# Kernel tuning notes

Measured on AMD Instinct MI355X. Metric: run time of the kernel, lower is better.

Reference implementation:

```python
import jax, jax.numpy as jnp
import numpy as np

B, N, C, H = 4, 2048, 1024, 16
HD = C // H  # head dim = 64


def setup_inputs() -> dict:
    key = jax.random.key(0)
    k1, k2, k3, k4 = jax.random.split(key, 4)
    x = jax.random.normal(k1, (B, N, C), dtype=jnp.float32)
    # nn.Linear(C, 3C, bias=False): weight [3C, C], y = x @ W.T
    w_qkv = jax.random.normal(k2, (3 * C, C), dtype=jnp.float32) * (C ** -0.5)
    # nn.Linear(C, C) with bias
    w_out = jax.random.normal(k3, (C, C), dtype=jnp.float32) * (C ** -0.5)
    b_out = jax.random.normal(k4, (C,), dtype=jnp.float32) * 0.01
    return {"x": x, "w_qkv": w_qkv, "w_out": w_out, "b_out": b_out}


def reference(x, w_qkv, w_out, b_out):
    scale = HD ** -0.5
    qkv = jnp.einsum('bnc,dc->bnd', x, w_qkv)  # [B, N, 3C]
    q, k, v = jnp.split(qkv, 3, axis=-1)
    # rearrange 'b n (h c) -> b h n c'
    def heads(t):
        return t.reshape(B, N, H, HD).transpose(0, 2, 1, 3)
    q, k, v = heads(q) * scale, heads(k), heads(v)
    scores = jnp.einsum('bhnc,bhmc->bhnm', q, k)  # [B, H, N, N]
    attn = jax.nn.softmax(scores, axis=-1)
    v_hat = jnp.einsum('bhnm,bhmc->bhnc', attn, v)
    out = v_hat.transpose(0, 2, 1, 3).reshape(B, N, C)  # 'b h n c -> b n (h c)'
    return jnp.einsum('bnc,dc->bnd', out, w_out) + b_out
```

## Files before the change

### kernel.cpp

```cpp
#include <hip/hip_runtime.h>

typedef unsigned short ushort_t;
typedef __attribute__((ext_vector_type(8))) short short8;
typedef __attribute__((ext_vector_type(4))) float f32x4;
typedef __attribute__((ext_vector_type(16))) float f32x16;
typedef __attribute__((ext_vector_type(4))) float float4v;
typedef __attribute__((ext_vector_type(4))) unsigned short ushortx4;
typedef __attribute__((ext_vector_type(4))) unsigned int uint4v;

#define AS1 __attribute__((address_space(1)))
#define AS3 __attribute__((address_space(3)))

#define B_ 4
#define N_ 2048
#define C_ 1024
#define H_ 16
#define HD_ 64
#define M_TOT 8192
#define N3_ 3072

#define QSCALE 0.18033688011112042f

__device__ __forceinline__ unsigned short f2bf(float f) {
    unsigned int u = __float_as_uint(f);
    u += 0x7fffu + ((u >> 16) & 1u);
    return (unsigned short)(u >> 16);
}

__global__ __launch_bounds__(256) void cast3_f32_bf16(const float* __restrict__ xa,
                                                      const float* __restrict__ xb,
                                                      const float* __restrict__ xc,
                                                      ushort_t* __restrict__ oa,
                                                      ushort_t* __restrict__ ob,
                                                      ushort_t* __restrict__ oc,
                                                      int n4a, int n4b, int n4c) {
    int i = blockIdx.x * blockDim.x + threadIdx.x;
    const int stride = gridDim.x * blockDim.x;
    const int tot = n4a + n4b + n4c;
    for (; i < tot; i += stride) {
        const float4v* src;
        ushortx4* dst;
        int j = i;
        if (j < n4a) { src = (const float4v*)xa; dst = (ushortx4*)oa; }
        else if ((j -= n4a) < n4b) { src = (const float4v*)xb; dst = (ushortx4*)ob; }
        else { j -= n4b; src = (const float4v*)xc; dst = (ushortx4*)oc; }
        float4v v = src[j];
        ushortx4 o;
        o[0] = f2bf(v[0]); o[1] = f2bf(v[1]); o[2] = f2bf(v[2]); o[3] = f2bf(v[3]);
        dst[j] = o;
    }
}


template <int EPI>
__global__ __launch_bounds__(512, 2) void gemm8p(const ushort_t* __restrict__ A,
                                                 const ushort_t* __restrict__ Bw,
                                                 ushort_t* __restrict__ o0,
                                                 ushort_t* __restrict__ o1,
                                                 ushort_t* __restrict__ o2,
                                                 float* __restrict__ outf,
                                                 const float* __restrict__ bias,
                                                 int K, int NBX) {
    extern __shared__ ushort_t smem[];
    const int tid = threadIdx.x;
    const int lane = tid & 63;
    const int wid = tid >> 6;
    const int l15 = lane & 15, lg = lane >> 4;
    const int wr = wid >> 1;
    const int wc = wid & 1;

    const int wg = blockIdx.x;
    const int id = (wg & 7) * ((int)gridDim.x >> 3) + (wg >> 3);
    const int by = id / NBX, bx = id - by * NBX;
    const int m0 = by * 256, n0 = bx * 128;

    const int koff = (((lane >> 4) ^ ((lane >> 1) & 3)) << 3);
    const int trow = tid >> 2;
    const int slotsrc = (tid & 3) ^ ((tid >> 3) & 3);

    auto stageA = [&](int q, int tt, int kh, int c) {
        const ushort_t* src = A + (size_t)(m0 + c * 128 + trow) * K + tt * 64 + kh * 32 +
                              slotsrc * 8;
        ushort_t* dst = smem + q * 24576 + kh * 8192 + c * 4096 + tid * 8;
        __builtin_amdgcn_global_load_lds((const AS1 void*)src, (AS3 void*)dst, 16, 0, 0);
    };
    auto stageB = [&](int q, int tt, int kh) {
        const ushort_t* src = Bw + (size_t)(n0 + trow) * K + tt * 64 + kh * 32 + slotsrc * 8;
        ushort_t* dst = smem + q * 24576 + 16384 + kh * 4096 + tid * 8;
        __builtin_amdgcn_global_load_lds((const AS1 void*)src, (AS3 void*)dst, 16, 0, 0);
    };

    f32x4 acc[4][4] = {};

    auto phase = [&](int p, int kh) {
        const ushort_t* Ab = smem + p * 24576 + kh * 8192;
        const ushort_t* Bb = smem + p * 24576 + 16384 + kh * 4096;
        short8 af[4], bfr[4];
#pragma unroll
        for (int rt = 0; rt < 4; ++rt)
            af[rt] = *(const short8*)(Ab + (wr * 64 + rt * 16 + l15) * 32 + koff);
#pragma unroll
        for (int ni = 0; ni < 4; ++ni)
            bfr[ni] = *(const short8*)(Bb + (wc * 64 + ni * 16 + l15) * 32 + koff);
        __builtin_amdgcn_s_setprio(1);
#pragma unroll
        for (int rt = 0; rt < 4; ++rt)
#pragma unroll
            for (int ni = 0; ni < 4; ++ni)
                acc[rt][ni] = __builtin_amdgcn_mfma_f32_16x16x32_bf16(af[rt], bfr[ni],
                                                                      acc[rt][ni], 0, 0, 0);
        __builtin_amdgcn_s_setprio(0);
    };

    stageA(0, 0, 0, 0); stageA(0, 0, 0, 1);
    stageA(0, 0, 1, 0); stageA(0, 0, 1, 1);
    stageB(0, 0, 0);    stageB(0, 0, 1);

    const int NT = K >> 6;
    for (int t = 0; t < NT; ++t) {
        const int p = t & 1, q = p ^ 1;
        if (t + 1 < NT) {
            stageA(q, t + 1, 0, 0); stageA(q, t + 1, 0, 1);
            __builtin_amdgcn_sched_barrier(0);
            asm volatile("s_waitcnt vmcnt(2)");
        } else {
            asm volatile("s_waitcnt vmcnt(0)");
        }
        __builtin_amdgcn_sched_barrier(0);
        __builtin_amdgcn_s_barrier();
        __builtin_amdgcn_sched_barrier(0);
        phase(p, 0);
        if (t + 1 < NT) {
            stageA(q, t + 1, 1, 0); stageA(q, t + 1, 1, 1);
            stageB(q, t + 1, 0);    stageB(q, t + 1, 1);
        }
        __builtin_amdgcn_sched_barrier(0);
        __builtin_amdgcn_s_barrier();
        __builtin_amdgcn_sched_barrier(0);
        phase(p, 1);
    }

    if (EPI == 0) {
        const int sel = bx >> 3;
#pragma unroll
        for (int mi = 0; mi < 4; ++mi) {
            const int r0 = m0 + wr * 64 + mi * 16 + lg * 4;
            const int b = r0 >> 11, n = r0 & 2047;
            const int blk = n >> 5, nlo = n & 31;
#pragma unroll
            for (int ni = 0; ni < 4; ++ni) {
                const int cq = (bx & 7) * 128 + wc * 64 + ni * 16 + l15;
                const int h = cq >> 6, hd = cq & 63;
                const int bh = b * H_ + h;
                f32x4 a = acc[mi][ni];
                if (sel == 2) {
                    size_t base = (((size_t)(bh * 64 + blk) * 2 + (hd >> 5)) * 2 +
                                   ((n >> 4) & 1)) * 512 +
                                  ((hd & 31) + ((n >> 3) & 1) * 32) * 8 + (n & 7);
                    ushortx4 pk;
#pragma unroll
                    for (int j = 0; j < 4; ++j) pk[j] = f2bf(a[j]);
                    *(ushortx4*)(&o2[base]) = pk;
                } else {
                    size_t base = ((size_t)(bh * 64 + blk) * 4 + (hd >> 4)) * 512 +
                                  (nlo + ((hd >> 3) & 1) * 32) * 8 + (hd & 7);
                    if (sel == 0) {
#pragma unroll
                        for (int j = 0; j < 4; ++j) o0[base + j * 8] = f2bf(a[j] * QSCALE);
                    } else {
#pragma unroll
                        for (int j = 0; j < 4; ++j) o1[base + j * 8] = f2bf(a[j]);
                    }
                }
            }
        }
    } else {
#pragma unroll
        for (int ni = 0; ni < 4; ++ni) {
            const int c = n0 + wc * 64 + ni * 16 + l15;
            const float bv = bias[c];
#pragma unroll
            for (int mi = 0; mi < 4; ++mi) {
                const int r0 = m0 + wr * 64 + mi * 16 + lg * 4;
                f32x4 a = acc[mi][ni];
#pragma unroll
                for (int j = 0; j < 4; ++j)
                    outf[(size_t)(r0 + j) * C_ + c] = a[j] + bv;
            }
        }
    }
}

__global__ __launch_bounds__(256, 2) void attn_fwd(const ushort_t* __restrict__ Qf,
                                                   const ushort_t* __restrict__ Kf,
                                                   const ushort_t* __restrict__ Vf,
                                                   ushort_t* __restrict__ Ov) {
    const int tid = threadIdx.x;
    const int lane = tid & 63;
    const int wid = tid >> 6;
    const int lc = lane & 31, lh = lane >> 5;

    const int wg = blockIdx.x;
    const int xcd = wg & 7, slot = wg >> 3;
    const int bh = xcd * 8 + (slot >> 3);
    const int qt = slot & 7;

    const ushort_t* qpb = Qf + (size_t)bh * N_ * HD_;
    const ushort_t* kpb = Kf + (size_t)bh * N_ * HD_;
    const ushort_t* vpb = Vf + (size_t)bh * N_ * HD_;

    const int qblk0 = qt * 8 + wid * 2;

    short8 qf[2][4];
#pragma unroll
    for (int qc = 0; qc < 2; ++qc)
#pragma unroll
        for (int ks = 0; ks < 4; ++ks)
            qf[qc][ks] = *(const short8*)(qpb + ((size_t)(qblk0 + qc) * 4 + ks) * 512 +
                                          lane * 8);

    f32x16 oacc[2][2] = {};
    float srun[2] = {0.f, 0.f};

    short8 kfA[4], kfB[4], vfA[4], vfB[4];
#pragma unroll
    for (int ks = 0; ks < 4; ++ks)
        kfA[ks] = *(const short8*)(kpb + (size_t)ks * 512 + lane * 8);
#pragma unroll
    for (int dt = 0; dt < 2; ++dt)
#pragma unroll
        for (int kb = 0; kb < 2; ++kb)
            vfA[dt * 2 + kb] = *(const short8*)(vpb + ((size_t)dt * 2 + kb) * 512 + lane * 8);

    auto iter = [&](short8(&kfu)[4], short8(&kfp)[4], short8(&vfu)[4], short8(&vfp)[4],
                    int t) {
        f32x16 sacc[2] = {};
        __builtin_amdgcn_s_setprio(1);
#pragma unroll
        for (int qc = 0; qc < 2; ++qc)
#pragma unroll
            for (int ks = 0; ks < 4; ++ks)
                sacc[qc] = __builtin_amdgcn_mfma_f32_32x32x16_bf16(kfu[ks], qf[qc][ks],
                                                                   sacc[qc], 0, 0, 0);
        __builtin_amdgcn_s_setprio(0);

        const int kvn = (t + 1) & 63;
#pragma unroll
        for (int ks = 0; ks < 4; ++ks)
            kfp[ks] = *(const short8*)(kpb + ((size_t)kvn * 4 + ks) * 512 + lane * 8);
#pragma unroll
        for (int dt = 0; dt < 2; ++dt)
#pragma unroll
            for (int kb = 0; kb < 2; ++kb)
                vfp[dt * 2 + kb] = *(const short8*)(vpb + (((size_t)kvn * 2 + dt) * 2 + kb) *
                                                    512 + lane * 8);

#pragma unroll
        for (int qc = 0; qc < 2; ++qc) {
            float p[16];
#pragma unroll
            for (int r = 0; r < 16; ++r) p[r] = __builtin_amdgcn_exp2f(sacc[qc][r]);
            float s01 = (p[0] + p[1]) + (p[2] + p[3]);
            float s23 = (p[4] + p[5]) + (p[6] + p[7]);
            float s45 = (p[8] + p[9]) + (p[10] + p[11]);
            float s67 = (p[12] + p[13]) + (p[14] + p[15]);
            srun[qc] += (s01 + s23) + (s45 + s67);

            unsigned pk[4][2];
#pragma unroll
            for (int r1 = 0; r1 < 4; ++r1)
#pragma unroll
                for (int c = 0; c < 2; ++c)
                    asm("v_cvt_pk_bf16_f32 %0, %1, %2"
                        : "=v"(pk[r1][c])
                        : "v"(p[4 * r1 + 2 * c]), "v"(p[4 * r1 + 2 * c + 1]));

            short8 pb[2];
#pragma unroll
            for (int kb = 0; kb < 2; ++kb) {
                unsigned a0 = pk[2 * kb][0], b0 = pk[2 * kb + 1][0];
                unsigned a1 = pk[2 * kb][1], b1 = pk[2 * kb + 1][1];
                asm("v_permlane32_swap_b32 %0, %1" : "+v"(a0), "+v"(b0));
                asm("v_permlane32_swap_b32 %0, %1" : "+v"(a1), "+v"(b1));
                uint4v w;
                w[0] = a0; w[1] = a1; w[2] = b0; w[3] = b1;
                pb[kb] = __builtin_bit_cast(short8, w);
            }

            __builtin_amdgcn_s_setprio(1);
#pragma unroll
            for (int dt = 0; dt < 2; ++dt)
#pragma unroll
                for (int kb = 0; kb < 2; ++kb)
                    oacc[qc][dt] = __builtin_amdgcn_mfma_f32_32x32x16_bf16(
                        vfu[dt * 2 + kb], pb[kb], oacc[qc][dt], 0, 0, 0);
            __builtin_amdgcn_s_setprio(0);
        }
    };

    for (int t2 = 0; t2 < 64; t2 += 2) {
        iter(kfA, kfB, vfA, vfB, t2);
        iter(kfB, kfA, vfB, vfA, t2 + 1);
    }

    const int b = bh >> 4, h = bh & 15;
#pragma unroll
    for (int qc = 0; qc < 2; ++qc) {
        float s = srun[qc];
        s += __shfl_xor(s, 32, 64);
        const float inv = 1.f / s;
        const int qg = (qblk0 + qc) * 32 + lc;
        ushort_t* orow = Ov + (size_t)(b * N_ + qg) * C_ + h * HD_;
#pragma unroll
        for (int dt = 0; dt < 2; ++dt)
#pragma unroll
            for (int r1 = 0; r1 < 4; ++r1) {
                ushortx4 pkv;
#pragma unroll
                for (int r0 = 0; r0 < 4; ++r0)
                    pkv[r0] = f2bf(oacc[qc][dt][4 * r1 + r0] * inv);
                *(ushortx4*)(orow + dt * 32 + r1 * 8 + lh * 4) = pkv;
            }
    }
}

extern "C" void kernel_launch(void* const* d_in, const int* in_sizes, int n_in,
                              void* d_out, int out_size, void* d_ws, size_t ws_size,
                              hipStream_t stream) {
    const float* x = (const float*)d_in[0];
    const float* wqkv = (const float*)d_in[1];
    const float* wout = (const float*)d_in[2];
    const float* bout = (const float*)d_in[3];
    float* out = (float*)d_out;

    ushort_t* ws = (ushort_t*)d_ws;
    const size_t XN = (size_t)M_TOT * C_;
    const size_t WQN = (size_t)N3_ * C_;
    const size_t WON = (size_t)C_ * C_;
    ushort_t* xbf = ws;
    ushort_t* wqkvb = xbf + XN;
    ushort_t* woutb = wqkvb + WQN;
    ushort_t* karr = woutb + WON;
    ushort_t* varr = karr + XN;
    ushort_t* qarr = varr + XN;
    ushort_t* vhat = xbf;

    cast3_f32_bf16<<<2048, 256, 0, stream>>>(x, wqkv, wout, xbf, wqkvb, woutb,
                                             (int)(XN / 4), (int)(WQN / 4), (int)(WON / 4));

    gemm8p<0><<<768, 512, 98304, stream>>>(xbf, wqkvb, qarr, karr, varr,
                                           nullptr, nullptr, C_, 24);
    attn_fwd<<<512, 256, 0, stream>>>(qarr, karr, varr, vhat);
    gemm8p<1><<<256, 512, 98304, stream>>>(vhat, woutb, nullptr, nullptr, nullptr,
                                           out, bout, C_, 8);
}
```

Baseline: 176.9 us.

## Fuse fp32-to-bf16 conversion of x into QKV GEMM A-tile staging

The QKV GEMM now reads fp32 x directly through register loads, converts it to bf16 with v_cvt_pk_bf16_f32, and writes swizzled tiles into LDS. This removes the separate cast pass over x and its bf16 round trip through global memory. The cast kernel now handles only the weights. In exchange the A operand no longer uses the async global_load_lds path: it reads twice the bytes per tile, each tile is loaded by all 24 N-blocks, and the pipeline has one barrier per k-step with a full vmcnt wait.

```diff
diff --git a/kernel.cpp b/kernel.cpp
--- a/kernel.cpp
+++ b/kernel.cpp
@@ -6,6 +6,7 @@
 typedef __attribute__((ext_vector_type(16))) float f32x16;
 typedef __attribute__((ext_vector_type(4))) float float4v;
 typedef __attribute__((ext_vector_type(4))) unsigned short ushortx4;
+typedef __attribute__((ext_vector_type(2))) unsigned int uint2v;
 typedef __attribute__((ext_vector_type(4))) unsigned int uint4v;
 
 #define AS1 __attribute__((address_space(1)))
@@ -27,22 +28,19 @@
     return (unsigned short)(u >> 16);
 }
 
-__global__ __launch_bounds__(256) void cast3_f32_bf16(const float* __restrict__ xa,
-                                                      const float* __restrict__ xb,
+__global__ __launch_bounds__(256) void cast2_f32_bf16(const float* __restrict__ xb,
                                                       const float* __restrict__ xc,
-                                                      ushort_t* __restrict__ oa,
                                                       ushort_t* __restrict__ ob,
                                                       ushort_t* __restrict__ oc,
-                                                      int n4a, int n4b, int n4c) {
+                                                      int n4b, int n4c) {
     int i = blockIdx.x * blockDim.x + threadIdx.x;
     const int stride = gridDim.x * blockDim.x;
-    const int tot = n4a + n4b + n4c;
+    const int tot = n4b + n4c;
     for (; i < tot; i += stride) {
         const float4v* src;
         ushortx4* dst;
         int j = i;
-        if (j < n4a) { src = (const float4v*)xa; dst = (ushortx4*)oa; }
-        else if ((j -= n4a) < n4b) { src = (const float4v*)xb; dst = (ushortx4*)ob; }
+        if (j < n4b) { src = (const float4v*)xb; dst = (ushortx4*)ob; }
         else { j -= n4b; src = (const float4v*)xc; dst = (ushortx4*)oc; }
         float4v v = src[j];
         ushortx4 o;
@@ -52,8 +50,8 @@
 }
 
 
-template <int EPI>
-__global__ __launch_bounds__(512, 2) void gemm8p(const ushort_t* __restrict__ A,
+template <int EPI, int AF32>
+__global__ __launch_bounds__(512, 2) void gemm8p(const void* __restrict__ Avoid,
                                                  const ushort_t* __restrict__ Bw,
                                                  ushort_t* __restrict__ o0,
                                                  ushort_t* __restrict__ o1,
@@ -62,6 +60,8 @@
                                                  const float* __restrict__ bias,
                                                  int K, int NBX) {
     extern __shared__ ushort_t smem[];
+    const ushort_t* A = (const ushort_t*)Avoid;
+    const float* Af = (const float*)Avoid;
     const int tid = threadIdx.x;
     const int lane = tid & 63;
     const int wid = tid >> 6;
@@ -78,7 +78,13 @@
     const int trow = tid >> 2;
     const int slotsrc = (tid & 3) ^ ((tid >> 3) & 3);
 
-    auto stageA = [&](int q, int tt, int kh, int c) {
+    const int wrow0 = wid * 32 + (lane >> 4);
+    const int acol = (lane & 15) * 4;
+    const int akh = (lane >> 3) & 1;
+    const int aslot = (lane & 7) >> 1;
+    const int ae = (lane & 1) * 4;
+
+    auto stageAbf = [&](int q, int tt, int kh, int c) {
         const ushort_t* src = A + (size_t)(m0 + c * 128 + trow) * K + tt * 64 + kh * 32 +
                               slotsrc * 8;
         ushort_t* dst = smem + q * 24576 + kh * 8192 + c * 4096 + tid * 8;
@@ -89,6 +95,14 @@
         ushort_t* dst = smem + q * 24576 + 16384 + kh * 4096 + tid * 8;
         __builtin_amdgcn_global_load_lds((const AS1 void*)src, (AS3 void*)dst, 16, 0, 0);
     };
+    auto writeA = [&](int q, const float4v& av, int j) {
+        uint2v w;
+        asm("v_cvt_pk_bf16_f32 %0, %1, %2" : "=v"(w[0]) : "v"(av[0]), "v"(av[1]));
+        asm("v_cvt_pk_bf16_f32 %0, %1, %2" : "=v"(w[1]) : "v"(av[2]), "v"(av[3]));
+        const int rj = wrow0 + j * 4;
+        const int dsv = aslot ^ ((rj >> 1) & 3);
+        *(uint2v*)(smem + q * 24576 + akh * 8192 + rj * 32 + dsv * 8 + ae) = w;
+    };
 
     f32x4 acc[4][4] = {};
 
@@ -112,32 +126,71 @@
         __builtin_amdgcn_s_setprio(0);
     };
 
-    stageA(0, 0, 0, 0); stageA(0, 0, 0, 1);
-    stageA(0, 0, 1, 0); stageA(0, 0, 1, 1);
-    stageB(0, 0, 0);    stageB(0, 0, 1);
-
     const int NT = K >> 6;
-    for (int t = 0; t < NT; ++t) {
-        const int p = t & 1, q = p ^ 1;
-        if (t + 1 < NT) {
-            stageA(q, t + 1, 0, 0); stageA(q, t + 1, 0, 1);
+
+    if constexpr (AF32) {
+        {
+            const float* as0 = Af + (size_t)(m0 + wrow0) * K + acol;
+            float4v av[8];
+#pragma unroll
+            for (int j = 0; j < 8; ++j) av[j] = *(const float4v*)(as0 + (size_t)(j * 4) * K);
+            stageB(0, 0, 0); stageB(0, 0, 1);
+#pragma unroll
+            for (int j = 0; j < 8; ++j) writeA(0, av[j], j);
+        }
+        __syncthreads();
+        for (int t = 0; t < NT; ++t) {
+            const int p = t & 1, q = p ^ 1;
+            const bool more = (t + 1 < NT);
+            float4v av[8];
+            if (more) {
+                const float* asrc = Af + (size_t)(m0 + wrow0) * K + (t + 1) * 64 + acol;
+#pragma unroll
+                for (int j = 0; j < 8; ++j)
+                    av[j] = *(const float4v*)(asrc + (size_t)(j * 4) * K);
+                stageB(q, t + 1, 0); stageB(q, t + 1, 1);
+            }
+            phase(p, 0);
+            if (more) {
+#pragma unroll
+                for (int j = 0; j < 8; ++j) writeA(q, av[j], j);
+            }
+            phase(p, 1);
+            if (more) {
+                __builtin_amdgcn_sched_barrier(0);
+                asm volatile("s_waitcnt vmcnt(0) lgkmcnt(0)");
+                __builtin_amdgcn_sched_barrier(0);
+                __builtin_amdgcn_s_barrier();
+                __builtin_amdgcn_sched_barrier(0);
+            }
+        }
+    } else {
+        stageAbf(0, 0, 0, 0); stageAbf(0, 0, 0, 1);
+        stageAbf(0, 0, 1, 0); stageAbf(0, 0, 1, 1);
+        stageB(0, 0, 0);      stageB(0, 0, 1);
+        __syncthreads();
+        for (int t = 0; t < NT; ++t) {
+            const int p = t & 1, q = p ^ 1;
+            if (t + 1 < NT) {
+                stageAbf(q, t + 1, 0, 0); stageAbf(q, t + 1, 0, 1);
+                __builtin_amdgcn_sched_barrier(0);
+                asm volatile("s_waitcnt vmcnt(2)");
+            } else {
+                asm volatile("s_waitcnt vmcnt(0)");
+            }
             __builtin_amdgcn_sched_barrier(0);
-            asm volatile("s_waitcnt vmcnt(2)");
-        } else {
-            asm volatile("s_waitcnt vmcnt(0)");
-        }
-        __builtin_amdgcn_sched_barrier(0);
-        __builtin_amdgcn_s_barrier();
-        __builtin_amdgcn_sched_barrier(0);
-        phase(p, 0);
-        if (t + 1 < NT) {
-            stageA(q, t + 1, 1, 0); stageA(q, t + 1, 1, 1);
-            stageB(q, t + 1, 0);    stageB(q, t + 1, 1);
-        }
-        __builtin_amdgcn_sched_barrier(0);
-        __builtin_amdgcn_s_barrier();
-        __builtin_amdgcn_sched_barrier(0);
-        phase(p, 1);
+            __builtin_amdgcn_s_barrier();
+            __builtin_amdgcn_sched_barrier(0);
+            phase(p, 0);
+            if (t + 1 < NT) {
+                stageAbf(q, t + 1, 1, 0); stageAbf(q, t + 1, 1, 1);
+                stageB(q, t + 1, 0);      stageB(q, t + 1, 1);
+            }
+            __builtin_amdgcn_sched_barrier(0);
+            __builtin_amdgcn_s_barrier();
+            __builtin_amdgcn_sched_barrier(0);
+            phase(p, 1);
+        }
     }
 
     if (EPI == 0) {
@@ -337,20 +390,19 @@
     const size_t XN = (size_t)M_TOT * C_;
     const size_t WQN = (size_t)N3_ * C_;
     const size_t WON = (size_t)C_ * C_;
-    ushort_t* xbf = ws;
-    ushort_t* wqkvb = xbf + XN;
+    ushort_t* wqkvb = ws;
     ushort_t* woutb = wqkvb + WQN;
     ushort_t* karr = woutb + WON;
     ushort_t* varr = karr + XN;
     ushort_t* qarr = varr + XN;
-    ushort_t* vhat = xbf;
-
-    cast3_f32_bf16<<<2048, 256, 0, stream>>>(x, wqkv, wout, xbf, wqkvb, woutb,
-                                             (int)(XN / 4), (int)(WQN / 4), (int)(WON / 4));
-
-    gemm8p<0><<<768, 512, 98304, stream>>>(xbf, wqkvb, qarr, karr, varr,
-                                           nullptr, nullptr, C_, 24);
+    ushort_t* vhat = qarr + XN;
+
+    cast2_f32_bf16<<<512, 256, 0, stream>>>(wqkv, wout, wqkvb, woutb,
+                                            (int)(WQN / 4), (int)(WON / 4));
+
+    gemm8p<0, 1><<<768, 512, 98304, stream>>>(x, wqkvb, qarr, karr, varr,
+                                              nullptr, nullptr, C_, 24);
     attn_fwd<<<512, 256, 0, stream>>>(qarr, karr, varr, vhat);
-    gemm8p<1><<<256, 512, 98304, stream>>>(vhat, woutb, nullptr, nullptr, nullptr,
-                                           out, bout, C_, 8);
+    gemm8p<1, 0><<<256, 512, 98304, stream>>>(vhat, woutb, nullptr, nullptr, nullptr,
+                                              out, bout, C_, 8);
 }
```

Result: slower. 196.7 us (+11.2%).

## Triple-buffer GEMM LDS stages with two-tile prefetch and finer interleaved phases

Applied to the files above, without the earlier changes.

Rewrites the bf16 GEMM main loop to use three LDS stages, prefetching two K-tiles ahead instead of one. Each K-tile is split into four sub-phases, with global-to-LDS loads interleaved between LDS fragment reads and MFMA groups. The aim is to hide global memory latency more fully. LDS use grows to 144 KB per block, which likely prevents two blocks from sharing a CU and reduces occupancy. The extra barriers also add synchronization cost.

```diff
diff --git a/kernel.cpp b/kernel.cpp
--- a/kernel.cpp
+++ b/kernel.cpp
@@ -53,7 +53,7 @@
 
 
 template <int EPI>
-__global__ __launch_bounds__(512, 2) void gemm8p(const ushort_t* __restrict__ A,
+__global__ __launch_bounds__(512, 2) void gemm8f(const ushort_t* __restrict__ A,
                                                  const ushort_t* __restrict__ Bw,
                                                  ushort_t* __restrict__ o0,
                                                  ushort_t* __restrict__ o1,
@@ -89,55 +89,124 @@
         ushort_t* dst = smem + q * 24576 + 16384 + kh * 4096 + tid * 8;
         __builtin_amdgcn_global_load_lds((const AS1 void*)src, (AS3 void*)dst, 16, 0, 0);
     };
+    auto stage6 = [&](int q, int tt) {
+        stageA(q, tt, 0, 0); stageA(q, tt, 0, 1);
+        stageA(q, tt, 1, 0); stageA(q, tt, 1, 1);
+        stageB(q, tt, 0);    stageB(q, tt, 1);
+    };
 
     f32x4 acc[4][4] = {};
 
-    auto phase = [&](int p, int kh) {
-        const ushort_t* Ab = smem + p * 24576 + kh * 8192;
-        const ushort_t* Bb = smem + p * 24576 + 16384 + kh * 4096;
-        short8 af[4], bfr[4];
-#pragma unroll
-        for (int rt = 0; rt < 4; ++rt)
-            af[rt] = *(const short8*)(Ab + (wr * 64 + rt * 16 + l15) * 32 + koff);
-#pragma unroll
-        for (int ni = 0; ni < 4; ++ni)
-            bfr[ni] = *(const short8*)(Bb + (wc * 64 + ni * 16 + l15) * 32 + koff);
-        __builtin_amdgcn_s_setprio(1);
-#pragma unroll
-        for (int rt = 0; rt < 4; ++rt)
-#pragma unroll
-            for (int ni = 0; ni < 4; ++ni)
-                acc[rt][ni] = __builtin_amdgcn_mfma_f32_16x16x32_bf16(af[rt], bfr[ni],
-                                                                      acc[rt][ni], 0, 0, 0);
-        __builtin_amdgcn_s_setprio(0);
-    };
-
-    stageA(0, 0, 0, 0); stageA(0, 0, 0, 1);
-    stageA(0, 0, 1, 0); stageA(0, 0, 1, 1);
-    stageB(0, 0, 0);    stageB(0, 0, 1);
+    auto rdA = [&](const ushort_t* base, int kh, int rt) -> short8 {
+        return *(const short8*)(base + kh * 8192 + (wr * 64 + rt * 16 + l15) * 32 + koff);
+    };
+    auto rdB = [&](const ushort_t* base, int kh, int ni) -> short8 {
+        return *(const short8*)(base + 16384 + kh * 4096 + (wc * 64 + ni * 16 + l15) * 32 +
+                                koff);
+    };
+
+    stage6(0, 0);
+    stage6(1, 1);
 
     const int NT = K >> 6;
+    int cur = 0;
     for (int t = 0; t < NT; ++t) {
-        const int p = t & 1, q = p ^ 1;
+        const int nxt = (cur + 2 >= 3) ? cur - 1 : cur + 2;
+        const bool pf = (t + 2 < NT);
+
         if (t + 1 < NT) {
-            stageA(q, t + 1, 0, 0); stageA(q, t + 1, 0, 1);
-            __builtin_amdgcn_sched_barrier(0);
-            asm volatile("s_waitcnt vmcnt(2)");
+            asm volatile("s_waitcnt vmcnt(6)");
         } else {
             asm volatile("s_waitcnt vmcnt(0)");
         }
         __builtin_amdgcn_sched_barrier(0);
         __builtin_amdgcn_s_barrier();
         __builtin_amdgcn_sched_barrier(0);
-        phase(p, 0);
-        if (t + 1 < NT) {
-            stageA(q, t + 1, 1, 0); stageA(q, t + 1, 1, 1);
-            stageB(q, t + 1, 0);    stageB(q, t + 1, 1);
-        }
-        __builtin_amdgcn_sched_barrier(0);
-        __builtin_amdgcn_s_barrier();
-        __builtin_amdgcn_sched_barrier(0);
-        phase(p, 1);
+
+        const ushort_t* base = smem + cur * 24576;
+        short8 a0, a1, bfr[4];
+
+        a0 = rdA(base, 0, 0); a1 = rdA(base, 0, 1);
+#pragma unroll
+        for (int ni = 0; ni < 4; ++ni) bfr[ni] = rdB(base, 0, ni);
+        if (pf) { stageA(nxt, t + 2, 0, 0); stageA(nxt, t + 2, 0, 1); }
+        __builtin_amdgcn_sched_barrier(0);
+        __builtin_amdgcn_s_barrier();
+        asm volatile("s_waitcnt lgkmcnt(0)");
+        __builtin_amdgcn_sched_barrier(0);
+        __builtin_amdgcn_s_setprio(1);
+#pragma unroll
+        for (int ni = 0; ni < 4; ++ni)
+            acc[0][ni] = __builtin_amdgcn_mfma_f32_16x16x32_bf16(a0, bfr[ni], acc[0][ni],
+                                                                 0, 0, 0);
+#pragma unroll
+        for (int ni = 0; ni < 4; ++ni)
+            acc[1][ni] = __builtin_amdgcn_mfma_f32_16x16x32_bf16(a1, bfr[ni], acc[1][ni],
+                                                                 0, 0, 0);
+        __builtin_amdgcn_s_setprio(0);
+        __builtin_amdgcn_sched_barrier(0);
+        __builtin_amdgcn_s_barrier();
+
+        a0 = rdA(base, 0, 2); a1 = rdA(base, 0, 3);
+        if (pf) stageB(nxt, t + 2, 0);
+        __builtin_amdgcn_sched_barrier(0);
+        __builtin_amdgcn_s_barrier();
+        asm volatile("s_waitcnt lgkmcnt(0)");
+        __builtin_amdgcn_sched_barrier(0);
+        __builtin_amdgcn_s_setprio(1);
+#pragma unroll
+        for (int ni = 0; ni < 4; ++ni)
+            acc[2][ni] = __builtin_amdgcn_mfma_f32_16x16x32_bf16(a0, bfr[ni], acc[2][ni],
+                                                                 0, 0, 0);
+#pragma unroll
+        for (int ni = 0; ni < 4; ++ni)
+            acc[3][ni] = __builtin_amdgcn_mfma_f32_16x16x32_bf16(a1, bfr[ni], acc[3][ni],
+                                                                 0, 0, 0);
+        __builtin_amdgcn_s_setprio(0);
+        __builtin_amdgcn_sched_barrier(0);
+        __builtin_amdgcn_s_barrier();
+
+        a0 = rdA(base, 1, 0); a1 = rdA(base, 1, 1);
+#pragma unroll
+        for (int ni = 0; ni < 4; ++ni) bfr[ni] = rdB(base, 1, ni);
+        if (pf) { stageA(nxt, t + 2, 1, 0); stageA(nxt, t + 2, 1, 1); }
+        __builtin_amdgcn_sched_barrier(0);
+        __builtin_amdgcn_s_barrier();
+        asm volatile("s_waitcnt lgkmcnt(0)");
+        __builtin_amdgcn_sched_barrier(0);
+        __builtin_amdgcn_s_setprio(1);
+#pragma unroll
+        for (int ni = 0; ni < 4; ++ni)
+            acc[0][ni] = __builtin_amdgcn_mfma_f32_16x16x32_bf16(a0, bfr[ni], acc[0][ni],
+                                                                 0, 0, 0);
+#pragma unroll
+        for (int ni = 0; ni < 4; ++ni)
+            acc[1][ni] = __builtin_amdgcn_mfma_f32_16x16x32_bf16(a1, bfr[ni], acc[1][ni],
+                                                                 0, 0, 0);
+        __builtin_amdgcn_s_setprio(0);
+        __builtin_amdgcn_sched_barrier(0);
+        __builtin_amdgcn_s_barrier();
+
+        a0 = rdA(base, 1, 2); a1 = rdA(base, 1, 3);
+        if (pf) stageB(nxt, t + 2, 1);
+        __builtin_amdgcn_sched_barrier(0);
+        __builtin_amdgcn_s_barrier();
+        asm volatile("s_waitcnt lgkmcnt(0)");
+        __builtin_amdgcn_sched_barrier(0);
+        __builtin_amdgcn_s_setprio(1);
+#pragma unroll
+        for (int ni = 0; ni < 4; ++ni)
+            acc[2][ni] = __builtin_amdgcn_mfma_f32_16x16x32_bf16(a0, bfr[ni], acc[2][ni],
+                                                                 0, 0, 0);
+#pragma unroll
+        for (int ni = 0; ni < 4; ++ni)
+            acc[3][ni] = __builtin_amdgcn_mfma_f32_16x16x32_bf16(a1, bfr[ni], acc[3][ni],
+                                                                 0, 0, 0);
+        __builtin_amdgcn_s_setprio(0);
+        __builtin_amdgcn_sched_barrier(0);
+        __builtin_amdgcn_s_barrier();
+
+        cur = (cur + 1 >= 3) ? 0 : cur + 1;
     }
 
     if (EPI == 0) {
@@ -154,22 +223,22 @@
                 const int bh = b * H_ + h;
                 f32x4 a = acc[mi][ni];
                 if (sel == 2) {
-                    size_t base = (((size_t)(bh * 64 + blk) * 2 + (hd >> 5)) * 2 +
-                                   ((n >> 4) & 1)) * 512 +
-                                  ((hd & 31) + ((n >> 3) & 1) * 32) * 8 + (n & 7);
+                    size_t base2 = (((size_t)(bh * 64 + blk) * 2 + (hd >> 5)) * 2 +
+                                    ((n >> 4) & 1)) * 512 +
+                                   ((hd & 31) + ((n >> 3) & 1) * 32) * 8 + (n & 7);
                     ushortx4 pk;
 #pragma unroll
                     for (int j = 0; j < 4; ++j) pk[j] = f2bf(a[j]);
-                    *(ushortx4*)(&o2[base]) = pk;
+                    *(ushortx4*)(&o2[base2]) = pk;
                 } else {
-                    size_t base = ((size_t)(bh * 64 + blk) * 4 + (hd >> 4)) * 512 +
-                                  (nlo + ((hd >> 3) & 1) * 32) * 8 + (hd & 7);
+                    size_t base2 = ((size_t)(bh * 64 + blk) * 4 + (hd >> 4)) * 512 +
+                                   (nlo + ((hd >> 3) & 1) * 32) * 8 + (hd & 7);
                     if (sel == 0) {
 #pragma unroll
-                        for (int j = 0; j < 4; ++j) o0[base + j * 8] = f2bf(a[j] * QSCALE);
+                        for (int j = 0; j < 4; ++j) o0[base2 + j * 8] = f2bf(a[j] * QSCALE);
                     } else {
 #pragma unroll
-                        for (int j = 0; j < 4; ++j) o1[base + j * 8] = f2bf(a[j]);
+                        for (int j = 0; j < 4; ++j) o1[base2 + j * 8] = f2bf(a[j]);
                     }
                 }
             }
@@ -348,9 +417,9 @@
     cast3_f32_bf16<<<2048, 256, 0, stream>>>(x, wqkv, wout, xbf, wqkvb, woutb,
                                              (int)(XN / 4), (int)(WQN / 4), (int)(WON / 4));
 
-    gemm8p<0><<<768, 512, 98304, stream>>>(xbf, wqkvb, qarr, karr, varr,
-                                           nullptr, nullptr, C_, 24);
+    gemm8f<0><<<768, 512, 147456, stream>>>(xbf, wqkvb, qarr, karr, varr,
+                                            nullptr, nullptr, C_, 24);
     attn_fwd<<<512, 256, 0, stream>>>(qarr, karr, varr, vhat);
-    gemm8p<1><<<256, 512, 98304, stream>>>(vhat, woutb, nullptr, nullptr, nullptr,
-                                           out, bout, C_, 8);
+    gemm8f<1><<<256, 512, 147456, stream>>>(vhat, woutb, nullptr, nullptr, nullptr,
+                                            out, bout, C_, 8);
 }
```

New measurement: 184.5 us. 4.3% more time.
